# Performance work log

Hardware: AMD Instinct MI355X
Metric: run time of the kernel (lower is better)

## Reference

```python
import jax, jax.numpy as jnp
import numpy as np

C_IN, C_OUT, K = 64, 64, 3
KK = K * K


def _conv3x3(x, w, b):
    # x: [B, Cin, H, W], w: [Cout, Cin, 3, 3], b: [Cout] or None. stride 1, pad 1.
    y = jax.lax.conv_general_dilated(
        x, w, window_strides=(1, 1), padding=((1, 1), (1, 1)),
        dimension_numbers=("NCHW", "OIHW", "NCHW"))
    if b is not None:
        y = y + b[None, :, None, None]
    return y


def _deform_conv2d(x, offset, mask, weight):
    # torchvision.ops.deform_conv2d with stride=1, pad=1, dilation=1, 1 offset group.
    # x: [B,C,H,W]; offset: [B,2*KK,H,W] (per-tap (dy,dx)); mask: [B,KK,H,W];
    # weight: [O,C,K,K]
    B, C, H, W = x.shape
    O = weight.shape[0]
    ky, kx = jnp.meshgrid(jnp.arange(K), jnp.arange(K), indexing="ij")
    hs = jnp.arange(H)
    ws = jnp.arange(W)
    # base sample positions per tap k=(ky*K+kx): [KK,H,W]
    base_y = (hs[:, None] - 1)[None] + ky.reshape(KK, 1, 1)
    base_x = (ws[None, :] - 1)[None] + kx.reshape(KK, 1, 1)
    off = offset.reshape(B, KK, 2, H, W)
    py = base_y[None].astype(x.dtype) + off[:, :, 0]  # [B,KK,H,W]
    px = base_x[None].astype(x.dtype) + off[:, :, 1]

    y0 = jnp.floor(py)
    x0 = jnp.floor(px)
    wy = py - y0  # bilinear fractional weights
    wx = px - x0
    y0i = y0.astype(jnp.int32)
    x0i = x0.astype(jnp.int32)

    imflat = x.reshape(B, C, H * W)

    def gather_b(im, idx):  # im: [C,HW], idx: [KK,H,W] -> [C,KK,H,W]
        return im[:, idx]

    val = jnp.zeros((B, C, KK, H, W), x.dtype)
    for dy, dx in ((0, 0), (0, 1), (1, 0), (1, 1)):
        yc = y0i + dy
        xc = x0i + dx
        valid = ((yc >= 0) & (yc < H) & (xc >= 0) & (xc < W)).astype(x.dtype)
        cw = (wy if dy else (1.0 - wy)) * (wx if dx else (1.0 - wx)) * valid
        idx = jnp.clip(yc, 0, H - 1) * W + jnp.clip(xc, 0, W - 1)
        g = jax.vmap(gather_b)(imflat, idx)  # [B,C,KK,H,W]
        val = val + cw[:, None] * g
    val = val * mask[:, None]  # modulation
    # contract 9-tap patches with conv weight
    return jnp.einsum("bckhw,ock->bohw", val, weight.reshape(O, C, KK))


def setup_inputs() -> dict:
    key = jax.random.key(0)
    ks = jax.random.split(key, 8)
    B, H, W = 4, 96, 96
    cin2 = 2 * C_IN + 2
    frame_i = jax.random.normal(ks[0], (B, C_IN, H, W), jnp.float32)
    frame_j = jax.random.normal(ks[1], (B, C_IN, H, W), jnp.float32)
    flow_ij = jax.random.normal(ks[2], (B, 2, H, W), jnp.float32)
    # small random weights so offsets are nonzero (zero-init would degenerate)
    w_off = jax.random.normal(ks[3], (2 * KK, cin2, K, K), jnp.float32) * 0.01
    b_off = jax.random.normal(ks[4], (2 * KK,), jnp.float32) * 0.1
    w_mod = jax.random.normal(ks[5], (KK, cin2, K, K), jnp.float32) * 0.01
    b_mod = jax.random.normal(ks[6], (KK,), jnp.float32) * 0.1
    w_reg = jax.random.normal(ks[7], (C_OUT, C_IN, K, K), jnp.float32) * (1.0 / np.sqrt(C_IN * KK))
    return {"frame_i": frame_i, "frame_j": frame_j, "flow_ij": flow_ij,
            "w_off": w_off, "b_off": b_off, "w_mod": w_mod, "b_mod": b_mod,
            "w_reg": w_reg}


def reference(frame_i, frame_j, flow_ij, w_off, b_off, w_mod, b_mod, w_reg):
    offset_input = jnp.concatenate([frame_i, frame_j, flow_ij], axis=1)
    offset = _conv3x3(offset_input, w_off, b_off)            # [B,2*KK,H,W]
    modulator = 2.0 * jax.nn.sigmoid(_conv3x3(offset_input, w_mod, b_mod))  # [B,KK,H,W]
    return _deform_conv2d(frame_j, offset, modulator, w_reg)
```

## Files before the change

kernel.cpp:

```cpp
#include <hip/hip_runtime.h>
#include <math.h>

#define BB   4
#define HH   96
#define WW   96
#define HW   (HH * WW)
#define CIN  64
#define COUT 64
#define C2B  192
#define NROW (BB * HW)
#define ZROW NROW
#define NSTRIP (NROW / 16)
#define BPX3 (NSTRIP / 8)
#define NA   (9 * 5 * 2 * 512)
#define NW   (9 * 2 * 4 * 512)
#define PXB2 (NROW / 32)
#define PWBLK 324
#define TSX  35
#define PR   55

typedef short v8s __attribute__((ext_vector_type(8)));
typedef float v4f __attribute__((ext_vector_type(4)));

__device__ __forceinline__ unsigned short f2bf(float f) {
    unsigned u = __float_as_uint(f);
    return (unsigned short)((u + 0x7FFFu + ((u >> 16) & 1u)) >> 16);
}
__device__ __forceinline__ unsigned pack2(float a, float b) {
    return (unsigned)f2bf(a) | ((unsigned)f2bf(b) << 16);
}
__device__ __forceinline__ unsigned bil2(unsigned a, unsigned b, unsigned c,
                                         unsigned d, float w00, float w01,
                                         float w10, float w11) {
    float lo = w00 * __uint_as_float(a << 16) + w01 * __uint_as_float(b << 16)
             + w10 * __uint_as_float(c << 16) + w11 * __uint_as_float(d << 16);
    float hi = w00 * __uint_as_float(a & 0xffff0000u)
             + w01 * __uint_as_float(b & 0xffff0000u)
             + w10 * __uint_as_float(c & 0xffff0000u)
             + w11 * __uint_as_float(d & 0xffff0000u);
    return pack2(lo, hi);
}

__global__ __launch_bounds__(256) void prep_kernel(
    const float* __restrict__ fi, const float* __restrict__ fj,
    const float* __restrict__ fl, const float* __restrict__ w_off,
    const float* __restrict__ w_mod, const float* __restrict__ w_reg,
    unsigned short* __restrict__ xt, unsigned short* __restrict__ wa2f,
    unsigned short* __restrict__ wb2f)
{
    int blk = blockIdx.x;
    if (blk < PXB2) {
        __shared__ __align__(16) unsigned tile[64 * TSX];
        int tid = threadIdx.x;
        int p = tid & 63, cg = tid >> 6;
        int u = blk >> 1, half = blk & 1;
        int r0 = u * 64;
        int b = r0 / HW;
        int hw = r0 - b * HW + p;
        uint4* dst = (uint4*)(xt + (size_t)r0 * C2B);
        if (half == 0) {
            const float* pi = fi + (size_t)b * CIN * HW + hw;
#pragma unroll
            for (int d = 0; d < 8; ++d) {
                int c = cg * 16 + 2 * d;
                tile[p * TSX + cg * 8 + d] =
                    pack2(pi[(size_t)c * HW], pi[(size_t)(c + 1) * HW]);
            }
            __syncthreads();
#pragma unroll
            for (int i = 0; i < 2; ++i) {
                int gq = i * 256 + tid;
                int rl = gq >> 3, c4 = gq & 7;
                const unsigned* s = &tile[rl * TSX + c4 * 4];
                uint4 v = {s[0], s[1], s[2], s[3]};
                dst[rl * 24 + c4] = v;
            }
        } else {
            const float* pj = fj + (size_t)b * CIN * HW + hw;
#pragma unroll
            for (int d = 0; d < 8; ++d) {
                int c = cg * 16 + 2 * d;
                tile[p * TSX + cg * 8 + d] =
                    pack2(pj[(size_t)c * HW], pj[(size_t)(c + 1) * HW]);
            }
            if (cg == 0) {
                const float* pf = fl + (size_t)b * 2 * HW + hw;
                tile[p * TSX + 32] = pack2(pf[0], pf[HW]);
            }
            __syncthreads();
#pragma unroll
            for (int i = 0; i < 4; ++i) {
                int gq = i * 256 + tid;
                int rl = gq >> 4, c4 = gq & 15;
                uint4 v = {0u, 0u, 0u, 0u};
                if (c4 < 8) {
                    const unsigned* s = &tile[rl * TSX + c4 * 4];
                    v.x = s[0]; v.y = s[1]; v.z = s[2]; v.w = s[3];
                } else if (c4 == 8) {
                    v.x = tile[rl * TSX + 32];
                }
                int pc4 = (c4 < 8) ? ((c4 & 3) * 2 + (c4 >> 2)) : c4;
                dst[rl * 24 + 8 + pc4] = v;
            }
        }
    } else if (blk < PXB2 + PWBLK) {
        int e = (blk - PXB2) * 256 + threadIdx.x;
        if (e < NA) {
            int t  = e / 5120;
            int r1 = e - t * 5120;
            int ks = r1 >> 10;
            int r2 = r1 & 1023;
            int nt = r2 >> 9;
            int l9 = r2 & 511;
            int l  = l9 >> 3, ee = l9 & 7;
            int m  = l & 15, g = l >> 4;
            int oc = nt * 16 + m;
            int ch = ks * 32 + g * 8 + ee;
            float v = 0.0f;
            if (oc < 27 && ch < 130) {
                if (oc < 18) v = w_off[((size_t)oc * 130 + ch) * 9 + t];
                else         v = w_mod[((size_t)(oc - 18) * 130 + ch) * 9 + t];
            }
            wa2f[e] = f2bf(v);
        } else {
            int e2 = e - NA;
            if (e2 < NW) {
                int k  = e2 >> 12;
                int r1 = e2 & 4095;
                int ks = r1 >> 11;
                int r2 = r1 & 2047;
                int nt = r2 >> 9;
                int l9 = r2 & 511;
                int l  = l9 >> 3, ee = l9 & 7;
                int m  = l & 15, g = l >> 4;
                int o  = nt * 16 + m;
                int c  = ks * 32 + g * 8 + ee;
                wb2f[e2] = f2bf(w_reg[((size_t)o * 64 + c) * 9 + k]);
            }
        }
    } else {
        if (threadIdx.x < 24) {
            uint4 z = {0u, 0u, 0u, 0u};
            ((uint4*)(xt + (size_t)ZROW * C2B))[threadIdx.x] = z;
        }
    }
}

__global__ __launch_bounds__(512, 4) void fused_kernel(
    const unsigned short* __restrict__ xt,
    const unsigned short* __restrict__ wa2f,
    const unsigned short* __restrict__ wb2f,
    const float* __restrict__ b_off, const float* __restrict__ b_mod,
    float* __restrict__ out)
{
    __shared__ __align__(16) unsigned char pool[32768];
    __shared__ __align__(16) float red1[8][8][64];
    __shared__ float lraw[16 * 28];

    uint4* patch4 = (uint4*)pool;
    float* red2   = (float*)pool;

    int l = threadIdx.x & 63;
    int wid = __builtin_amdgcn_readfirstlane(threadIdx.x >> 6);
    int m = l & 15, g = l >> 4;
    int strip = (blockIdx.x & 7) * BPX3 + (blockIdx.x >> 3);
    int b = strip / (HW / 16);
    int hw0 = (strip - b * (HW / 16)) * 16;
    int hw = hw0 + m;
    int x = hw % WW, y = hw / WW;
    int y0b = hw0 / WW, x0b = hw0 - y0b * WW;

#pragma unroll
    for (int i = 0; i < 3; ++i) {
        int item = i * 512 + threadIdx.x;
        if (item < 1080) {
            int run = item / 360;
            int rem = item - run * 360;
            int r18 = rem / 20;
            int c8  = rem - r18 * 20;
            int yy = y0b + run - 1;
            int xx = x0b - 1 + r18;
            bool ok = ((unsigned)yy < HH) && ((unsigned)xx < WW);
            uint4 v = {0u, 0u, 0u, 0u};
            if (ok)
                v = ((const uint4*)(xt + (size_t)(b * HW + yy * WW + xx) * C2B))[c8];
            patch4[c8 * PR + run * 18 + r18] = v;
        }
    }
    __syncthreads();

    v4f acc0 = {0.f, 0.f, 0.f, 0.f};
    v4f acc1 = {0.f, 0.f, 0.f, 0.f};
    {
        int nu = (wid < 5) ? 6 : 5;
#pragma unroll
        for (int i = 0; i < 6; ++i) {
            if (i < nu) {
                int u = wid + 8 * i;
                int t = u / 5, ks = u - 5 * t;
                int r = (t / 3) * 18 + (t % 3) + m;
                int c8 = (ks == 0) ? g : (ks == 1) ? 4 + g
                       : (ks == 2) ? 8 + 2 * g : (ks == 3) ? 9 + 2 * g
                       : 16 + g;
                v8s a = *(const v8s*)&patch4[c8 * PR + r];
                const unsigned short* wp =
                    wa2f + ((size_t)(u * 2)) * 512 + l * 8;
                v8s b0 = *(const v8s*)(wp);
                v8s b1 = *(const v8s*)(wp + 512);
                acc0 = __builtin_amdgcn_mfma_f32_16x16x32_bf16(a, b0, acc0, 0, 0, 0);
                acc1 = __builtin_amdgcn_mfma_f32_16x16x32_bf16(a, b1, acc1, 0, 0, 0);
            }
        }
    }

    {
#pragma unroll
        for (int j = 0; j < 4; ++j) red1[wid][j][l] = acc0[j];
#pragma unroll
        for (int j = 0; j < 4; ++j) red1[wid][4 + j][l] = acc1[j];
    }
    __syncthreads();

    {
        int j = wid;
        float v = 0.f;
#pragma unroll
        for (int sw = 0; sw < 8; ++sw) v += red1[sw][j][l];
        int r = j & 3;
        int oc = (j < 4) ? m : 16 + m;
        int pos = g * 4 + r;
        if (oc < 18) {
            lraw[pos * 28 + oc] = v + b_off[oc];
        } else if (oc < 27) {
            lraw[pos * 28 + oc] =
                2.0f / (1.0f + __expf(-(v + b_mod[oc - 18])));
        }
    }
    __syncthreads();

    v4f acc[4];
#pragma unroll
    for (int nt = 0; nt < 4; ++nt) acc[nt] = (v4f){0.f, 0.f, 0.f, 0.f};

    const unsigned short* rowb =
        xt + (size_t)(b * HW) * C2B + 64 + g * 16;

    auto do_tap = [&](int k) {
        int ky = k / 3, kx = k - 3 * ky;
        float dy = lraw[m * 28 + 2 * k];
        float dx = lraw[m * 28 + 2 * k + 1];
        float mm = lraw[m * 28 + 18 + k];

        float py = (float)(y - 1 + ky) + dy;
        float px = (float)(x - 1 + kx) + dx;
        float fy = floorf(py), fx = floorf(px);
        int   y0 = (int)fy,    x0 = (int)fx;
        float wy = py - fy,    wx = px - fx;
        int   y1 = y0 + 1,     x1 = x0 + 1;

        bool y0v = (y0 >= 0) && (y0 < HH);
        bool y1v = (y1 >= 0) && (y1 < HH);
        bool x0v = (x0 >= 0) && (x0 < WW);
        bool x1v = (x1 >= 0) && (x1 < WW);

        float w00 = (1.f - wy) * (1.f - wx) * ((y0v && x0v) ? mm : 0.f);
        float w01 = (1.f - wy) * wx         * ((y0v && x1v) ? mm : 0.f);
        float w10 = wy * (1.f - wx)         * ((y1v && x0v) ? mm : 0.f);
        float w11 = wy * wx                 * ((y1v && x1v) ? mm : 0.f);

        int y0c = min(max(y0, 0), HH - 1), y1c = min(max(y1, 0), HH - 1);
        int x0c = min(max(x0, 0), WW - 1), x1c = min(max(x1, 0), WW - 1);
        const unsigned short* r00 = rowb + (size_t)(y0c * WW + x0c) * C2B;
        const unsigned short* r01 = rowb + (size_t)(y0c * WW + x1c) * C2B;
        const unsigned short* r10 = rowb + (size_t)(y1c * WW + x0c) * C2B;
        const unsigned short* r11 = rowb + (size_t)(y1c * WW + x1c) * C2B;

        uint4 a00 = *(const uint4*)(r00);
        uint4 a01 = *(const uint4*)(r01);
        uint4 a10 = *(const uint4*)(r10);
        uint4 a11 = *(const uint4*)(r11);
        uint4 c00 = *(const uint4*)(r00 + 8);
        uint4 c01 = *(const uint4*)(r01 + 8);
        uint4 c10 = *(const uint4*)(r10 + 8);
        uint4 c11 = *(const uint4*)(r11 + 8);

        uint4 ov0, ov1;
        ov0.x = bil2(a00.x, a01.x, a10.x, a11.x, w00, w01, w10, w11);
        ov0.y = bil2(a00.y, a01.y, a10.y, a11.y, w00, w01, w10, w11);
        ov0.z = bil2(a00.z, a01.z, a10.z, a11.z, w00, w01, w10, w11);
        ov0.w = bil2(a00.w, a01.w, a10.w, a11.w, w00, w01, w10, w11);
        ov1.x = bil2(c00.x, c01.x, c10.x, c11.x, w00, w01, w10, w11);
        ov1.y = bil2(c00.y, c01.y, c10.y, c11.y, w00, w01, w10, w11);
        ov1.z = bil2(c00.z, c01.z, c10.z, c11.z, w00, w01, w10, w11);
        ov1.w = bil2(c00.w, c01.w, c10.w, c11.w, w00, w01, w10, w11);
        v8s af0 = __builtin_bit_cast(v8s, ov0);
        v8s af1 = __builtin_bit_cast(v8s, ov1);

#pragma unroll
        for (int nt = 0; nt < 4; ++nt) {
            const unsigned short* wp0 =
                wb2f + ((size_t)((k * 2 + 0) * 4 + nt)) * 512 + l * 8;
            const unsigned short* wp1 =
                wb2f + ((size_t)((k * 2 + 1) * 4 + nt)) * 512 + l * 8;
            v8s bb0 = *(const v8s*)wp0;
            v8s bb1 = *(const v8s*)wp1;
            acc[nt] = __builtin_amdgcn_mfma_f32_16x16x32_bf16(af0, bb0, acc[nt], 0, 0, 0);
            acc[nt] = __builtin_amdgcn_mfma_f32_16x16x32_bf16(af1, bb1, acc[nt], 0, 0, 0);
        }
    };

    do_tap(wid);
    if (wid == 7) do_tap(8);

    {
#pragma unroll
        for (int nt = 0; nt < 4; ++nt)
#pragma unroll
            for (int r = 0; r < 4; ++r)
                red2[((size_t)wid * 16 + nt * 4 + r) * 64 + l] = acc[nt][r];
    }
    __syncthreads();
    {
        int nt = wid >> 1, r0 = (wid & 1) * 2;
        float v0 = 0.f, v1 = 0.f;
#pragma unroll
        for (int sw = 0; sw < 8; ++sw) {
            v0 += red2[((size_t)sw * 16 + nt * 4 + r0) * 64 + l];
            v1 += red2[((size_t)sw * 16 + nt * 4 + r0 + 1) * 64 + l];
        }
        float* op = out + ((size_t)(b * COUT + nt * 16 + m)) * HW
                  + hw0 + g * 4 + r0;
        float2 s2 = {v0, v1};
        *(float2*)op = s2;
    }
}

extern "C" void kernel_launch(void* const* d_in, const int* in_sizes, int n_in,
                              void* d_out, int out_size, void* d_ws, size_t ws_size,
                              hipStream_t stream)
{
    const float* frame_i = (const float*)d_in[0];
    const float* frame_j = (const float*)d_in[1];
    const float* flow_ij = (const float*)d_in[2];
    const float* w_off   = (const float*)d_in[3];
    const float* b_off   = (const float*)d_in[4];
    const float* w_mod   = (const float*)d_in[5];
    const float* b_mod   = (const float*)d_in[6];
    const float* w_reg   = (const float*)d_in[7];
    float* out = (float*)d_out;

    unsigned short* xt   = (unsigned short*)d_ws;
    unsigned short* wa2f = xt + (size_t)(NROW + 1) * C2B;
    unsigned short* wb2f = wa2f + NA;

    prep_kernel<<<PXB2 + PWBLK + 1, 256, 0, stream>>>(
        frame_i, frame_j, flow_ij, w_off, w_mod, w_reg, xt, wa2f, wb2f);

    fused_kernel<<<NSTRIP, 512, 0, stream>>>(
        xt, wa2f, wb2f, b_off, b_mod, out);
}
```

Before: 123.4 us.

## Process 32 pixels per block so each weight fragment feeds two MFMAs

Each workgroup of the fused kernel now handles 32 consecutive pixels in one image row, half as many blocks as before. The offset/modulator conv patch staged in LDS now covers a 3x34 window, and every loaded weight B-fragment is reused for two M=16 tiles in both the offset conv and the deformable contraction. The aim is to cut global weight loads and halo re-fetching per pixel and to amortize block setup and barriers. In exchange it uses more LDS, accumulator registers and reduction buffers per block, which may lower occupancy, and it adds an extra barrier before the final reduction.

After: 126.6 us. +2.6%, slower.

```diff
diff --git a/kernel.cpp b/kernel.cpp
--- a/kernel.cpp
+++ b/kernel.cpp
@@ -10,14 +10,15 @@
 #define C2B  192
 #define NROW (BB * HW)
 #define ZROW NROW
-#define NSTRIP (NROW / 16)
-#define BPX3 (NSTRIP / 8)
+#define MPB  32
+#define NBLK (NROW / MPB)
+#define BPX4 (NBLK / 8)
 #define NA   (9 * 5 * 2 * 512)
 #define NW   (9 * 2 * 4 * 512)
 #define PXB2 (NROW / 32)
 #define PWBLK 324
 #define TSX  35
-#define PR   55
+#define PR2  103
 
 typedef short v8s __attribute__((ext_vector_type(8)));
 typedef float v4f __attribute__((ext_vector_type(4)));
@@ -153,44 +154,47 @@
     const float* __restrict__ b_off, const float* __restrict__ b_mod,
     float* __restrict__ out)
 {
-    __shared__ __align__(16) unsigned char pool[32768];
-    __shared__ __align__(16) float red1[8][8][64];
-    __shared__ float lraw[16 * 28];
+    __shared__ __align__(16) unsigned char pool[32960];
+    __shared__ __align__(16) float red1buf[8192];
+    __shared__ float lraw[32 * 28];
 
     uint4* patch4 = (uint4*)pool;
-    float* red2   = (float*)pool;
+    float* red2q0 = (float*)pool;
+    float* red2q1 = red1buf;
 
     int l = threadIdx.x & 63;
     int wid = __builtin_amdgcn_readfirstlane(threadIdx.x >> 6);
     int m = l & 15, g = l >> 4;
-    int strip = (blockIdx.x & 7) * BPX3 + (blockIdx.x >> 3);
-    int b = strip / (HW / 16);
-    int hw0 = (strip - b * (HW / 16)) * 16;
-    int hw = hw0 + m;
-    int x = hw % WW, y = hw / WW;
-    int y0b = hw0 / WW, x0b = hw0 - y0b * WW;
-
-#pragma unroll
-    for (int i = 0; i < 3; ++i) {
+    int blkid = (blockIdx.x & 7) * BPX4 + (blockIdx.x >> 3);
+    int b = blkid / (HW / MPB);
+    int rem = blkid - b * (HW / MPB);
+    int y = rem / 3;
+    int x0b = (rem - y * 3) * 32;
+    int hw0 = y * WW + x0b;
+
+#pragma unroll
+    for (int i = 0; i < 4; ++i) {
         int item = i * 512 + threadIdx.x;
-        if (item < 1080) {
-            int run = item / 360;
-            int rem = item - run * 360;
-            int r18 = rem / 20;
-            int c8  = rem - r18 * 20;
-            int yy = y0b + run - 1;
-            int xx = x0b - 1 + r18;
+        if (item < 2040) {
+            int e   = item / 20;
+            int c8  = item - e * 20;
+            int run = e / 34;
+            int r34 = e - run * 34;
+            int yy = y + run - 1;
+            int xx = x0b - 1 + r34;
             bool ok = ((unsigned)yy < HH) && ((unsigned)xx < WW);
             uint4 v = {0u, 0u, 0u, 0u};
             if (ok)
                 v = ((const uint4*)(xt + (size_t)(b * HW + yy * WW + xx) * C2B))[c8];
-            patch4[c8 * PR + run * 18 + r18] = v;
-        }
-    }
-    __syncthreads();
-
-    v4f acc0 = {0.f, 0.f, 0.f, 0.f};
-    v4f acc1 = {0.f, 0.f, 0.f, 0.f};
+            patch4[c8 * PR2 + e] = v;
+        }
+    }
+    __syncthreads();
+
+    v4f acc00 = {0.f, 0.f, 0.f, 0.f};
+    v4f acc01 = {0.f, 0.f, 0.f, 0.f};
+    v4f acc10 = {0.f, 0.f, 0.f, 0.f};
+    v4f acc11 = {0.f, 0.f, 0.f, 0.f};
     {
         int nu = (wid < 5) ? 6 : 5;
 #pragma unroll
@@ -198,103 +202,123 @@
             if (i < nu) {
                 int u = wid + 8 * i;
                 int t = u / 5, ks = u - 5 * t;
-                int r = (t / 3) * 18 + (t % 3) + m;
+                int run = t / 3, kx = t - 3 * run;
                 int c8 = (ks == 0) ? g : (ks == 1) ? 4 + g
                        : (ks == 2) ? 8 + 2 * g : (ks == 3) ? 9 + 2 * g
                        : 16 + g;
-                v8s a = *(const v8s*)&patch4[c8 * PR + r];
+                int base = c8 * PR2 + run * 34 + kx;
+                v8s a0 = *(const v8s*)&patch4[base + m];
+                v8s a1 = *(const v8s*)&patch4[base + 16 + m];
                 const unsigned short* wp =
                     wa2f + ((size_t)(u * 2)) * 512 + l * 8;
                 v8s b0 = *(const v8s*)(wp);
                 v8s b1 = *(const v8s*)(wp + 512);
-                acc0 = __builtin_amdgcn_mfma_f32_16x16x32_bf16(a, b0, acc0, 0, 0, 0);
-                acc1 = __builtin_amdgcn_mfma_f32_16x16x32_bf16(a, b1, acc1, 0, 0, 0);
-            }
-        }
-    }
-
-    {
-#pragma unroll
-        for (int j = 0; j < 4; ++j) red1[wid][j][l] = acc0[j];
-#pragma unroll
-        for (int j = 0; j < 4; ++j) red1[wid][4 + j][l] = acc1[j];
-    }
-    __syncthreads();
-
-    {
-        int j = wid;
-        float v = 0.f;
-#pragma unroll
-        for (int sw = 0; sw < 8; ++sw) v += red1[sw][j][l];
-        int r = j & 3;
-        int oc = (j < 4) ? m : 16 + m;
-        int pos = g * 4 + r;
-        if (oc < 18) {
-            lraw[pos * 28 + oc] = v + b_off[oc];
-        } else if (oc < 27) {
-            lraw[pos * 28 + oc] =
-                2.0f / (1.0f + __expf(-(v + b_mod[oc - 18])));
-        }
-    }
-    __syncthreads();
-
-    v4f acc[4];
-#pragma unroll
-    for (int nt = 0; nt < 4; ++nt) acc[nt] = (v4f){0.f, 0.f, 0.f, 0.f};
+                acc00 = __builtin_amdgcn_mfma_f32_16x16x32_bf16(a0, b0, acc00, 0, 0, 0);
+                acc01 = __builtin_amdgcn_mfma_f32_16x16x32_bf16(a0, b1, acc01, 0, 0, 0);
+                acc10 = __builtin_amdgcn_mfma_f32_16x16x32_bf16(a1, b0, acc10, 0, 0, 0);
+                acc11 = __builtin_amdgcn_mfma_f32_16x16x32_bf16(a1, b1, acc11, 0, 0, 0);
+            }
+        }
+    }
+
+    {
+        float* rb = red1buf;
+#pragma unroll
+        for (int j = 0; j < 4; ++j) {
+            rb[((wid * 2 + 0) * 8 + j) * 64 + l]     = acc00[j];
+            rb[((wid * 2 + 0) * 8 + 4 + j) * 64 + l] = acc01[j];
+            rb[((wid * 2 + 1) * 8 + j) * 64 + l]     = acc10[j];
+            rb[((wid * 2 + 1) * 8 + 4 + j) * 64 + l] = acc11[j];
+        }
+    }
+    __syncthreads();
+
+    {
+#pragma unroll
+        for (int ss = 0; ss < 2; ++ss) {
+            int s = wid * 2 + ss;
+            int q = s >> 3, j = s & 7;
+            float v = 0.f;
+#pragma unroll
+            for (int sw = 0; sw < 8; ++sw)
+                v += red1buf[((sw * 2 + q) * 8 + j) * 64 + l];
+            int r = j & 3;
+            int oc = (j < 4) ? m : 16 + m;
+            int pos = q * 16 + g * 4 + r;
+            if (oc < 18) {
+                lraw[pos * 28 + oc] = v + b_off[oc];
+            } else if (oc < 27) {
+                lraw[pos * 28 + oc] =
+                    2.0f / (1.0f + __expf(-(v + b_mod[oc - 18])));
+            }
+        }
+    }
+    __syncthreads();
+
+    v4f acc2[2][4];
+#pragma unroll
+    for (int q = 0; q < 2; ++q)
+#pragma unroll
+        for (int nt = 0; nt < 4; ++nt) acc2[q][nt] = (v4f){0.f, 0.f, 0.f, 0.f};
 
     const unsigned short* rowb =
         xt + (size_t)(b * HW) * C2B + 64 + g * 16;
 
     auto do_tap = [&](int k) {
         int ky = k / 3, kx = k - 3 * ky;
-        float dy = lraw[m * 28 + 2 * k];
-        float dx = lraw[m * 28 + 2 * k + 1];
-        float mm = lraw[m * 28 + 18 + k];
-
-        float py = (float)(y - 1 + ky) + dy;
-        float px = (float)(x - 1 + kx) + dx;
-        float fy = floorf(py), fx = floorf(px);
-        int   y0 = (int)fy,    x0 = (int)fx;
-        float wy = py - fy,    wx = px - fx;
-        int   y1 = y0 + 1,     x1 = x0 + 1;
-
-        bool y0v = (y0 >= 0) && (y0 < HH);
-        bool y1v = (y1 >= 0) && (y1 < HH);
-        bool x0v = (x0 >= 0) && (x0 < WW);
-        bool x1v = (x1 >= 0) && (x1 < WW);
-
-        float w00 = (1.f - wy) * (1.f - wx) * ((y0v && x0v) ? mm : 0.f);
-        float w01 = (1.f - wy) * wx         * ((y0v && x1v) ? mm : 0.f);
-        float w10 = wy * (1.f - wx)         * ((y1v && x0v) ? mm : 0.f);
-        float w11 = wy * wx                 * ((y1v && x1v) ? mm : 0.f);
-
-        int y0c = min(max(y0, 0), HH - 1), y1c = min(max(y1, 0), HH - 1);
-        int x0c = min(max(x0, 0), WW - 1), x1c = min(max(x1, 0), WW - 1);
-        const unsigned short* r00 = rowb + (size_t)(y0c * WW + x0c) * C2B;
-        const unsigned short* r01 = rowb + (size_t)(y0c * WW + x1c) * C2B;
-        const unsigned short* r10 = rowb + (size_t)(y1c * WW + x0c) * C2B;
-        const unsigned short* r11 = rowb + (size_t)(y1c * WW + x1c) * C2B;
-
-        uint4 a00 = *(const uint4*)(r00);
-        uint4 a01 = *(const uint4*)(r01);
-        uint4 a10 = *(const uint4*)(r10);
-        uint4 a11 = *(const uint4*)(r11);
-        uint4 c00 = *(const uint4*)(r00 + 8);
-        uint4 c01 = *(const uint4*)(r01 + 8);
-        uint4 c10 = *(const uint4*)(r10 + 8);
-        uint4 c11 = *(const uint4*)(r11 + 8);
-
-        uint4 ov0, ov1;
-        ov0.x = bil2(a00.x, a01.x, a10.x, a11.x, w00, w01, w10, w11);
-        ov0.y = bil2(a00.y, a01.y, a10.y, a11.y, w00, w01, w10, w11);
-        ov0.z = bil2(a00.z, a01.z, a10.z, a11.z, w00, w01, w10, w11);
-        ov0.w = bil2(a00.w, a01.w, a10.w, a11.w, w00, w01, w10, w11);
-        ov1.x = bil2(c00.x, c01.x, c10.x, c11.x, w00, w01, w10, w11);
-        ov1.y = bil2(c00.y, c01.y, c10.y, c11.y, w00, w01, w10, w11);
-        ov1.z = bil2(c00.z, c01.z, c10.z, c11.z, w00, w01, w10, w11);
-        ov1.w = bil2(c00.w, c01.w, c10.w, c11.w, w00, w01, w10, w11);
-        v8s af0 = __builtin_bit_cast(v8s, ov0);
-        v8s af1 = __builtin_bit_cast(v8s, ov1);
+        v8s af[2][2];
+#pragma unroll
+        for (int q = 0; q < 2; ++q) {
+            int pos = q * 16 + m;
+            float dy = lraw[pos * 28 + 2 * k];
+            float dx = lraw[pos * 28 + 2 * k + 1];
+            float mm = lraw[pos * 28 + 18 + k];
+
+            float py = (float)(y - 1 + ky) + dy;
+            float px = (float)(x0b + pos - 1 + kx) + dx;
+            float fy = floorf(py), fx = floorf(px);
+            int   y0 = (int)fy,    x0 = (int)fx;
+            float wy = py - fy,    wx = px - fx;
+            int   y1 = y0 + 1,     x1 = x0 + 1;
+
+            bool y0v = (y0 >= 0) && (y0 < HH);
+            bool y1v = (y1 >= 0) && (y1 < HH);
+            bool x0v = (x0 >= 0) && (x0 < WW);
+            bool x1v = (x1 >= 0) && (x1 < WW);
+
+            float w00 = (1.f - wy) * (1.f - wx) * ((y0v && x0v) ? mm : 0.f);
+            float w01 = (1.f - wy) * wx         * ((y0v && x1v) ? mm : 0.f);
+            float w10 = wy * (1.f - wx)         * ((y1v && x0v) ? mm : 0.f);
+            float w11 = wy * wx                 * ((y1v && x1v) ? mm : 0.f);
+
+            int y0c = min(max(y0, 0), HH - 1), y1c = min(max(y1, 0), HH - 1);
+            int x0c = min(max(x0, 0), WW - 1), x1c = min(max(x1, 0), WW - 1);
+            const unsigned short* r00 = rowb + (size_t)(y0c * WW + x0c) * C2B;
+            const unsigned short* r01 = rowb + (size_t)(y0c * WW + x1c) * C2B;
+            const unsigned short* r10 = rowb + (size_t)(y1c * WW + x0c) * C2B;
+            const unsigned short* r11 = rowb + (size_t)(y1c * WW + x1c) * C2B;
+
+            uint4 a00 = *(const uint4*)(r00);
+            uint4 a01 = *(const uint4*)(r01);
+            uint4 a10 = *(const uint4*)(r10);
+            uint4 a11 = *(const uint4*)(r11);
+            uint4 c00 = *(const uint4*)(r00 + 8);
+            uint4 c01 = *(const uint4*)(r01 + 8);
+            uint4 c10 = *(const uint4*)(r10 + 8);
+            uint4 c11 = *(const uint4*)(r11 + 8);
+
+            uint4 ov0, ov1;
+            ov0.x = bil2(a00.x, a01.x, a10.x, a11.x, w00, w01, w10, w11);
+            ov0.y = bil2(a00.y, a01.y, a10.y, a11.y, w00, w01, w10, w11);
+            ov0.z = bil2(a00.z, a01.z, a10.z, a11.z, w00, w01, w10, w11);
+            ov0.w = bil2(a00.w, a01.w, a10.w, a11.w, w00, w01, w10, w11);
+            ov1.x = bil2(c00.x, c01.x, c10.x, c11.x, w00, w01, w10, w11);
+            ov1.y = bil2(c00.y, c01.y, c10.y, c11.y, w00, w01, w10, w11);
+            ov1.z = bil2(c00.z, c01.z, c10.z, c11.z, w00, w01, w10, w11);
+            ov1.w = bil2(c00.w, c01.w, c10.w, c11.w, w00, w01, w10, w11);
+            af[q][0] = __builtin_bit_cast(v8s, ov0);
+            af[q][1] = __builtin_bit_cast(v8s, ov1);
+        }
 
 #pragma unroll
         for (int nt = 0; nt < 4; ++nt) {
@@ -304,34 +328,43 @@
                 wb2f + ((size_t)((k * 2 + 1) * 4 + nt)) * 512 + l * 8;
             v8s bb0 = *(const v8s*)wp0;
             v8s bb1 = *(const v8s*)wp1;
-            acc[nt] = __builtin_amdgcn_mfma_f32_16x16x32_bf16(af0, bb0, acc[nt], 0, 0, 0);
-            acc[nt] = __builtin_amdgcn_mfma_f32_16x16x32_bf16(af1, bb1, acc[nt], 0, 0, 0);
+            acc2[0][nt] = __builtin_amdgcn_mfma_f32_16x16x32_bf16(af[0][0], bb0, acc2[0][nt], 0, 0, 0);
+            acc2[0][nt] = __builtin_amdgcn_mfma_f32_16x16x32_bf16(af[0][1], bb1, acc2[0][nt], 0, 0, 0);
+            acc2[1][nt] = __builtin_amdgcn_mfma_f32_16x16x32_bf16(af[1][0], bb0, acc2[1][nt], 0, 0, 0);
+            acc2[1][nt] = __builtin_amdgcn_mfma_f32_16x16x32_bf16(af[1][1], bb1, acc2[1][nt], 0, 0, 0);
         }
     };
 
     do_tap(wid);
     if (wid == 7) do_tap(8);
 
+    __syncthreads();
     {
 #pragma unroll
         for (int nt = 0; nt < 4; ++nt)
 #pragma unroll
-            for (int r = 0; r < 4; ++r)
-                red2[((size_t)wid * 16 + nt * 4 + r) * 64 + l] = acc[nt][r];
+            for (int r = 0; r < 4; ++r) {
+                red2q0[((size_t)wid * 16 + nt * 4 + r) * 64 + l] = acc2[0][nt][r];
+                red2q1[((size_t)wid * 16 + nt * 4 + r) * 64 + l] = acc2[1][nt][r];
+            }
     }
     __syncthreads();
     {
         int nt = wid >> 1, r0 = (wid & 1) * 2;
-        float v0 = 0.f, v1 = 0.f;
+        float v0 = 0.f, v1 = 0.f, u0 = 0.f, u1 = 0.f;
 #pragma unroll
         for (int sw = 0; sw < 8; ++sw) {
-            v0 += red2[((size_t)sw * 16 + nt * 4 + r0) * 64 + l];
-            v1 += red2[((size_t)sw * 16 + nt * 4 + r0 + 1) * 64 + l];
+            v0 += red2q0[((size_t)sw * 16 + nt * 4 + r0) * 64 + l];
+            v1 += red2q0[((size_t)sw * 16 + nt * 4 + r0 + 1) * 64 + l];
+            u0 += red2q1[((size_t)sw * 16 + nt * 4 + r0) * 64 + l];
+            u1 += red2q1[((size_t)sw * 16 + nt * 4 + r0 + 1) * 64 + l];
         }
         float* op = out + ((size_t)(b * COUT + nt * 16 + m)) * HW
                   + hw0 + g * 4 + r0;
-        float2 s2 = {v0, v1};
-        *(float2*)op = s2;
+        float2 s0 = {v0, v1};
+        float2 s1 = {u0, u1};
+        *(float2*)op = s0;
+        *(float2*)(op + 16) = s1;
     }
 }
 
@@ -356,6 +389,6 @@
     prep_kernel<<<PXB2 + PWBLK + 1, 256, 0, stream>>>(
         frame_i, frame_j, flow_ij, w_off, w_mod, w_reg, xt, wa2f, wb2f);
 
-    fused_kernel<<<NSTRIP, 512, 0, stream>>>(
+    fused_kernel<<<NBLK, 512, 0, stream>>>(
         xt, wa2f, wb2f, b_off, b_mod, out);
 }
```
